# Kernel tuning notes

Measured on AMD Instinct MI355X. Metric: run time of the kernel, lower is better.

Reference implementation:

```python
import jax, jax.numpy as jnp
import numpy as np

N, E, D_NLP, D_EMB = 100000, 500000, 768, 128


def setup_inputs() -> dict:
    key = jax.random.key(0)
    ks = jax.random.split(key, 6)
    z = jax.random.normal(ks[0], (N, D_EMB), jnp.float32)
    z0 = jax.random.normal(ks[1], (N, D_NLP), jnp.float32)
    edge_index = jax.random.randint(ks[2], (2, E), 0, N)
    w0 = jax.random.normal(ks[3], (D_EMB, D_NLP), jnp.float32) / np.sqrt(D_NLP)
    prelu_a = jnp.full((1,), 0.25, jnp.float32)  # torch PReLU default init
    w1 = jax.random.normal(ks[4], (1, 3 * D_EMB), jnp.float32) / np.sqrt(3 * D_EMB)
    b1 = jnp.zeros((1,), jnp.float32)
    return {"z": z, "z0": z0, "edge_index": edge_index, "w0": w0,
            "prelu_a": prelu_a, "w1": w1, "b1": b1}


def reference(z, z0, edge_index, w0, prelu_a, w1, b1):
    # qid = elementwise max of the two endpoint rows, shifted to start at 0
    qid = jnp.max(edge_index[0:2], axis=0)
    qid = qid - qid.min()
    # lin0 (no bias) + PReLU with scalar slope
    h = z0[qid] @ w0.T                       # [E, D_EMB]
    x0 = jnp.where(h >= 0, h, prelu_a[0] * h)
    emb1 = z[edge_index[0]]                  # [E, D_EMB]
    emb2 = z[edge_index[1]]                  # [E, D_EMB]
    # lin1(concat([emb1, emb2, x0])) == sum of three matvecs; avoids a [E, 3*D] concat
    w1a, w1b, w1c = w1[0, :D_EMB], w1[0, D_EMB:2 * D_EMB], w1[0, 2 * D_EMB:]
    out = emb1 @ w1a + emb2 @ w1b + x0 @ w1c + b1[0]
    return out  # [E]
```

## Files before the change

kernel.cpp:

```cpp
#include <hip/hip_runtime.h>
#include <hip/hip_bf16.h>
#include <stdint.h>

#define D_EMB 128
#define D_NLP 768
#define BM 64
#define BK 64
#define NKC (D_NLP / BK)

typedef __attribute__((ext_vector_type(8))) short bf16x8;
typedef __attribute__((ext_vector_type(4))) float f32x4;
typedef __attribute__((ext_vector_type(8))) unsigned short u16x8;

__device__ __forceinline__ unsigned short f2bf(float f) {
  unsigned u = __builtin_bit_cast(unsigned, f);
  u += 0x7fffu + ((u >> 16) & 1u);
  return (unsigned short)(u >> 16);
}

__global__ void kw(const float* __restrict__ w0, unsigned short* __restrict__ w0s,
                   int* __restrict__ mn) {
  if (blockIdx.x == 0 && threadIdx.x == 0) mn[0] = 0x7fffffff;
  int t = blockIdx.x * 256 + threadIdx.x;
  if (t >= (D_EMB * D_NLP) / 8) return;
  int u = t & 7, row = (t >> 3) & 127, kc = t >> 10;
  const float4* src = (const float4*)(w0 + (size_t)row * D_NLP + kc * BK + ((u ^ (row & 7)) * 8));
  float4 v0 = src[0], v1 = src[1];
  u16x8 o;
  o[0] = f2bf(v0.x); o[1] = f2bf(v0.y); o[2] = f2bf(v0.z); o[3] = f2bf(v0.w);
  o[4] = f2bf(v1.x); o[5] = f2bf(v1.y); o[6] = f2bf(v1.z); o[7] = f2bf(v1.w);
  *(u16x8*)(w0s + (size_t)t * 8) = o;
}

__global__ void km(const int* __restrict__ ei, int E, int* __restrict__ mn) {
  int t = blockIdx.x * blockDim.x + threadIdx.x;
  int stride = gridDim.x * blockDim.x;
  int m = 0x7fffffff;
  for (int e = t; e < E; e += stride) {
    int a = ei[e], b = ei[E + e];
    int q = a > b ? a : b;
    m = q < m ? q : m;
  }
  #pragma unroll
  for (int off = 32; off; off >>= 1) {
    int o = __shfl_xor(m, off);
    m = o < m ? o : m;
  }
  if ((threadIdx.x & 63) == 0) atomicMin(mn, m);
}

__global__ __launch_bounds__(256) void kc(
    const float* __restrict__ z0, const float* __restrict__ z,
    const unsigned short* __restrict__ w0s, const float* __restrict__ w1,
    const float* __restrict__ prelu_a, float* __restrict__ sv,
    float* __restrict__ ta, float* __restrict__ tb, int N) {
  __shared__ unsigned short Bb[2][D_EMB * BK];

  const int tid = threadIdx.x;
  const int lane = tid & 63;
  const int wave = tid >> 6;
  const int r0 = blockIdx.x * BM;
  const int kg = lane >> 4;
  const int myrow = r0 + wave * 16 + (lane & 15);
  const int arow_g = min(myrow, N - 1);
  const float* aBase = z0 + (size_t)arow_g * D_NLP + kg * 8;

  f32x4 acc[8];
  #pragma unroll
  for (int c = 0; c < 8; ++c) acc[c] = (f32x4){0.f, 0.f, 0.f, 0.f};

  float4 fa[4];
  bf16x8 af[2];

  auto loadA = [&](int t) {
    const float4* p0 = (const float4*)(aBase + t * BK);
    const float4* p1 = (const float4*)(aBase + t * BK + 32);
    fa[0] = p0[0]; fa[1] = p0[1]; fa[2] = p1[0]; fa[3] = p1[1];
  };

  auto cvtA = [&]() {
    u16x8 v;
    v[0] = f2bf(fa[0].x); v[1] = f2bf(fa[0].y); v[2] = f2bf(fa[0].z); v[3] = f2bf(fa[0].w);
    v[4] = f2bf(fa[1].x); v[5] = f2bf(fa[1].y); v[6] = f2bf(fa[1].z); v[7] = f2bf(fa[1].w);
    af[0] = __builtin_bit_cast(bf16x8, v);
    v[0] = f2bf(fa[2].x); v[1] = f2bf(fa[2].y); v[2] = f2bf(fa[2].z); v[3] = f2bf(fa[2].w);
    v[4] = f2bf(fa[3].x); v[5] = f2bf(fa[3].y); v[6] = f2bf(fa[3].z); v[7] = f2bf(fa[3].w);
    af[1] = __builtin_bit_cast(bf16x8, v);
  };

  auto stageB = [&](int t, int buf) {
    const unsigned short* g = w0s + (size_t)t * (D_EMB * BK) + (size_t)tid * 8;
    #pragma unroll
    for (int p = 0; p < 4; ++p) {
      __builtin_amdgcn_global_load_lds(
          (const __attribute__((address_space(1))) void*)(g + p * 256 * 8),
          (__attribute__((address_space(3))) void*)&Bb[buf][(wave * 64 + p * 256) * 8],
          16, 0, 0);
    }
  };

  auto compute = [&](int buf) {
    #pragma unroll
    for (int ks = 0; ks < 2; ++ks) {
      #pragma unroll
      for (int c = 0; c < 8; ++c) {
        int brow = c * 16 + (lane & 15);
        bf16x8 bfr = *(const bf16x8*)&Bb[buf][(brow * 8 + ((ks * 4 + kg) ^ (brow & 7))) * 8];
        acc[c] = __builtin_amdgcn_mfma_f32_16x16x32_bf16(af[ks], bfr, acc[c], 0, 0, 0);
      }
    }
  };

  loadA(0);
  stageB(0, 0);
  __syncthreads();
  for (int t = 0; t < NKC; ++t) {
    cvtA();
    if (t + 1 < NKC) { loadA(t + 1); stageB(t + 1, (t + 1) & 1); }
    compute(t & 1);
    __syncthreads();
  }

  float ap = prelu_a[0];
  float ssum[4] = {0.f, 0.f, 0.f, 0.f};
  #pragma unroll
  for (int c = 0; c < 8; ++c) {
    float wc = w1[2 * D_EMB + c * 16 + (lane & 15)];
    #pragma unroll
    for (int i = 0; i < 4; ++i) {
      float h = acc[c][i];
      float x = h >= 0.f ? h : ap * h;
      ssum[i] += x * wc;
    }
  }
  #pragma unroll
  for (int off = 1; off < 16; off <<= 1) {
    #pragma unroll
    for (int i = 0; i < 4; ++i) ssum[i] += __shfl_xor(ssum[i], off);
  }
  if ((lane & 15) == 0) {
    int rbase = r0 + wave * 16 + (lane >> 4) * 4;
    #pragma unroll
    for (int i = 0; i < 4; ++i) {
      int r = rbase + i;
      if (r < N) sv[r] = ssum[i];
    }
  }

  {
    const float* zp = z + (size_t)arow_g * D_EMB + kg * 32;
    const float4* wa4 = (const float4*)(w1 + kg * 32);
    const float4* wb4 = (const float4*)(w1 + D_EMB + kg * 32);
    float pa = 0.f, pb = 0.f;
    #pragma unroll
    for (int i = 0; i < 8; ++i) {
      float4 zv = ((const float4*)zp)[i];
      float4 wa = wa4[i];
      float4 wb = wb4[i];
      pa += zv.x * wa.x + zv.y * wa.y + zv.z * wa.z + zv.w * wa.w;
      pb += zv.x * wb.x + zv.y * wb.y + zv.z * wb.z + zv.w * wb.w;
    }
    pa += __shfl_xor(pa, 16); pa += __shfl_xor(pa, 32);
    pb += __shfl_xor(pb, 16); pb += __shfl_xor(pb, 32);
    if (kg == 0 && myrow < N) { ta[myrow] = pa; tb[myrow] = pb; }
  }
}

__global__ void kd(const int* __restrict__ ei, const int* __restrict__ mn,
                   const float* __restrict__ ta, const float* __restrict__ tb,
                   const float* __restrict__ sv, const float* __restrict__ b1,
                   float* __restrict__ out, int E) {
  int e = blockIdx.x * blockDim.x + threadIdx.x;
  if (e >= E) return;
  int i0 = ei[e], i1 = ei[E + e];
  int q = (i0 > i1 ? i0 : i1) - mn[0];
  out[e] = ta[i0] + tb[i1] + sv[q] + b1[0];
}

extern "C" void kernel_launch(void* const* d_in, const int* in_sizes, int n_in,
                              void* d_out, int out_size, void* d_ws, size_t ws_size,
                              hipStream_t stream) {
  const float* z  = (const float*)d_in[0];
  const float* z0 = (const float*)d_in[1];
  const int*   ei = (const int*)d_in[2];
  const float* w0 = (const float*)d_in[3];
  const float* pa = (const float*)d_in[4];
  const float* w1 = (const float*)d_in[5];
  const float* b1 = (const float*)d_in[6];
  float* out = (float*)d_out;
  const int N = in_sizes[0] / D_EMB;
  const int E = in_sizes[2] / 2;

  char* ws = (char*)d_ws;
  int* mn = (int*)ws;
  unsigned short* w0s = (unsigned short*)(ws + 256);
  float* ta = (float*)(ws + 256 + 196608);
  float* tb = ta + N;
  float* sv = tb + N;

  kw<<<(D_EMB * D_NLP / 8 + 255) / 256, 256, 0, stream>>>(w0, w0s, mn);
  km<<<256, 256, 0, stream>>>(ei, E, mn);
  kc<<<(N + BM - 1) / BM, 256, 0, stream>>>(z0, z, w0s, w1, pa, sv, ta, tb, N);
  kd<<<(E + 255) / 256, 256, 0, stream>>>(ei, mn, ta, tb, sv, b1, out, E);
}
```

Baseline: 127.5 us.

## Read B fragments directly from global/L2 and triple-buffer A loads in registers

```diff
diff --git a/kernel.cpp b/kernel.cpp
--- a/kernel.cpp
+++ b/kernel.cpp
@@ -18,18 +18,17 @@
   return (unsigned short)(u >> 16);
 }
 
-__global__ void kw(const float* __restrict__ w0, unsigned short* __restrict__ w0s,
+__global__ void kw(const float* __restrict__ w0, unsigned short* __restrict__ w0b,
                    int* __restrict__ mn) {
-  if (blockIdx.x == 0 && threadIdx.x == 0) mn[0] = 0x7fffffff;
   int t = blockIdx.x * 256 + threadIdx.x;
+  if (t == 0) mn[0] = 0x7fffffff;
   if (t >= (D_EMB * D_NLP) / 8) return;
-  int u = t & 7, row = (t >> 3) & 127, kc = t >> 10;
-  const float4* src = (const float4*)(w0 + (size_t)row * D_NLP + kc * BK + ((u ^ (row & 7)) * 8));
+  const float4* src = (const float4*)(w0 + (size_t)t * 8);
   float4 v0 = src[0], v1 = src[1];
   u16x8 o;
   o[0] = f2bf(v0.x); o[1] = f2bf(v0.y); o[2] = f2bf(v0.z); o[3] = f2bf(v0.w);
   o[4] = f2bf(v1.x); o[5] = f2bf(v1.y); o[6] = f2bf(v1.z); o[7] = f2bf(v1.w);
-  *(u16x8*)(w0s + (size_t)t * 8) = o;
+  *(u16x8*)(w0b + (size_t)t * 8) = o;
 }
 
 __global__ void km(const int* __restrict__ ei, int E, int* __restrict__ mn) {
@@ -51,81 +50,60 @@
 
 __global__ __launch_bounds__(256) void kc(
     const float* __restrict__ z0, const float* __restrict__ z,
-    const unsigned short* __restrict__ w0s, const float* __restrict__ w1,
+    const unsigned short* __restrict__ w0b, const float* __restrict__ w1,
     const float* __restrict__ prelu_a, float* __restrict__ sv,
     float* __restrict__ ta, float* __restrict__ tb, int N) {
-  __shared__ unsigned short Bb[2][D_EMB * BK];
-
   const int tid = threadIdx.x;
   const int lane = tid & 63;
   const int wave = tid >> 6;
-  const int r0 = blockIdx.x * BM;
   const int kg = lane >> 4;
-  const int myrow = r0 + wave * 16 + (lane & 15);
+  const int col = lane & 15;
+  const int myrow = blockIdx.x * BM + wave * 16 + col;
   const int arow_g = min(myrow, N - 1);
   const float* aBase = z0 + (size_t)arow_g * D_NLP + kg * 8;
+  const unsigned short* bBase = w0b + (size_t)col * D_NLP + kg * 8;
 
   f32x4 acc[8];
   #pragma unroll
   for (int c = 0; c < 8; ++c) acc[c] = (f32x4){0.f, 0.f, 0.f, 0.f};
 
-  float4 fa[4];
-  bf16x8 af[2];
+  float4 fa[3][4];
 
-  auto loadA = [&](int t) {
+  auto loadA = [&](float4* f, int t) {
     const float4* p0 = (const float4*)(aBase + t * BK);
     const float4* p1 = (const float4*)(aBase + t * BK + 32);
-    fa[0] = p0[0]; fa[1] = p0[1]; fa[2] = p1[0]; fa[3] = p1[1];
+    f[0] = p0[0]; f[1] = p0[1]; f[2] = p1[0]; f[3] = p1[1];
   };
 
-  auto cvtA = [&]() {
+  loadA(fa[0], 0);
+  loadA(fa[1], 1);
+
+  #pragma unroll
+  for (int t = 0; t < NKC; ++t) {
+    if (t + 2 < NKC) loadA(fa[(t + 2) % 3], t + 2);
+    const float4* f = fa[t % 3];
     u16x8 v;
-    v[0] = f2bf(fa[0].x); v[1] = f2bf(fa[0].y); v[2] = f2bf(fa[0].z); v[3] = f2bf(fa[0].w);
-    v[4] = f2bf(fa[1].x); v[5] = f2bf(fa[1].y); v[6] = f2bf(fa[1].z); v[7] = f2bf(fa[1].w);
-    af[0] = __builtin_bit_cast(bf16x8, v);
-    v[0] = f2bf(fa[2].x); v[1] = f2bf(fa[2].y); v[2] = f2bf(fa[2].z); v[3] = f2bf(fa[2].w);
-    v[4] = f2bf(fa[3].x); v[5] = f2bf(fa[3].y); v[6] = f2bf(fa[3].z); v[7] = f2bf(fa[3].w);
-    af[1] = __builtin_bit_cast(bf16x8, v);
-  };
-
-  auto stageB = [&](int t, int buf) {
-    const unsigned short* g = w0s + (size_t)t * (D_EMB * BK) + (size_t)tid * 8;
+    v[0] = f2bf(f[0].x); v[1] = f2bf(f[0].y); v[2] = f2bf(f[0].z); v[3] = f2bf(f[0].w);
+    v[4] = f2bf(f[1].x); v[5] = f2bf(f[1].y); v[6] = f2bf(f[1].z); v[7] = f2bf(f[1].w);
+    bf16x8 af0 = __builtin_bit_cast(bf16x8, v);
+    v[0] = f2bf(f[2].x); v[1] = f2bf(f[2].y); v[2] = f2bf(f[2].z); v[3] = f2bf(f[2].w);
+    v[4] = f2bf(f[3].x); v[5] = f2bf(f[3].y); v[6] = f2bf(f[3].z); v[7] = f2bf(f[3].w);
+    bf16x8 af1 = __builtin_bit_cast(bf16x8, v);
     #pragma unroll
-    for (int p = 0; p < 4; ++p) {
-      __builtin_amdgcn_global_load_lds(
-          (const __attribute__((address_space(1))) void*)(g + p * 256 * 8),
-          (__attribute__((address_space(3))) void*)&Bb[buf][(wave * 64 + p * 256) * 8],
-          16, 0, 0);
+    for (int c = 0; c < 8; ++c) {
+      const unsigned short* bp = bBase + (size_t)c * 16 * D_NLP + t * BK;
+      bf16x8 b0 = *(const bf16x8*)bp;
+      bf16x8 b1 = *(const bf16x8*)(bp + 32);
+      acc[c] = __builtin_amdgcn_mfma_f32_16x16x32_bf16(af0, b0, acc[c], 0, 0, 0);
+      acc[c] = __builtin_amdgcn_mfma_f32_16x16x32_bf16(af1, b1, acc[c], 0, 0, 0);
     }
-  };
-
-  auto compute = [&](int buf) {
-    #pragma unroll
-    for (int ks = 0; ks < 2; ++ks) {
-      #pragma unroll
-      for (int c = 0; c < 8; ++c) {
-        int brow = c * 16 + (lane & 15);
-        bf16x8 bfr = *(const bf16x8*)&Bb[buf][(brow * 8 + ((ks * 4 + kg) ^ (brow & 7))) * 8];
-        acc[c] = __builtin_amdgcn_mfma_f32_16x16x32_bf16(af[ks], bfr, acc[c], 0, 0, 0);
-      }
-    }
-  };
-
-  loadA(0);
-  stageB(0, 0);
-  __syncthreads();
-  for (int t = 0; t < NKC; ++t) {
-    cvtA();
-    if (t + 1 < NKC) { loadA(t + 1); stageB(t + 1, (t + 1) & 1); }
-    compute(t & 1);
-    __syncthreads();
   }
 
   float ap = prelu_a[0];
   float ssum[4] = {0.f, 0.f, 0.f, 0.f};
   #pragma unroll
   for (int c = 0; c < 8; ++c) {
-    float wc = w1[2 * D_EMB + c * 16 + (lane & 15)];
+    float wc = w1[2 * D_EMB + c * 16 + col];
     #pragma unroll
     for (int i = 0; i < 4; ++i) {
       float h = acc[c][i];
@@ -138,8 +116,8 @@
     #pragma unroll
     for (int i = 0; i < 4; ++i) ssum[i] += __shfl_xor(ssum[i], off);
   }
-  if ((lane & 15) == 0) {
-    int rbase = r0 + wave * 16 + (lane >> 4) * 4;
+  if (col == 0) {
+    int rbase = blockIdx.x * BM + wave * 16 + kg * 4;
     #pragma unroll
     for (int i = 0; i < 4; ++i) {
       int r = rbase + i;
@@ -193,13 +171,13 @@
 
   char* ws = (char*)d_ws;
   int* mn = (int*)ws;
-  unsigned short* w0s = (unsigned short*)(ws + 256);
+  unsigned short* w0b = (unsigned short*)(ws + 256);
   float* ta = (float*)(ws + 256 + 196608);
   float* tb = ta + N;
   float* sv = tb + N;
 
-  kw<<<(D_EMB * D_NLP / 8 + 255) / 256, 256, 0, stream>>>(w0, w0s, mn);
+  kw<<<(D_EMB * D_NLP / 8 + 255) / 256, 256, 0, stream>>>(w0, w0b, mn);
   km<<<256, 256, 0, stream>>>(ei, E, mn);
-  kc<<<(N + BM - 1) / BM, 256, 0, stream>>>(z0, z, w0s, w1, pa, sv, ta, tb, N);
+  kc<<<(N + BM - 1) / BM, 256, 0, stream>>>(z0, z, w0b, w1, pa, sv, ta, tb, N);
   kd<<<(E + 255) / 256, 256, 0, stream>>>(ei, mn, ta, tb, sv, b1, out, E);
 }
```

After: 243.7 us. 1.91x slower.
